# Optimization experiments

Measured on AMD Instinct MI355X. Metric: run time of the kernel, lower is better.

Reference implementation:

```python
import jax, jax.numpy as jnp
import numpy as np

N_NODES = 100000
N_EDGES = 3200000
IN_DIM = 128
OUT_DIM = 64
ITERS = 2


def setup_inputs() -> dict:
    key = jax.random.key(0)
    k1, k2, k3, k4, k5, k6 = jax.random.split(key, 6)
    feature = jax.random.normal(k1, (N_NODES, IN_DIM), dtype=jnp.float32)
    src = jax.random.randint(k2, (N_EDGES,), 0, N_NODES, dtype=jnp.int32)
    dst = jax.random.randint(k3, (N_EDGES,), 0, N_NODES, dtype=jnp.int32)
    # Kaiming-ish scaling for stability
    W_lin = jax.random.normal(k4, (IN_DIM, OUT_DIM), dtype=jnp.float32) / np.sqrt(IN_DIM)
    W_d1 = jax.random.normal(k5, (OUT_DIM, OUT_DIM), dtype=jnp.float32) / np.sqrt(OUT_DIM)
    W_d2 = jax.random.normal(k6, (OUT_DIM, OUT_DIM), dtype=jnp.float32) / np.sqrt(OUT_DIM)
    return {"feature": feature, "src": src, "dst": dst,
            "W_lin": W_lin, "W_d1": W_d1, "W_d2": W_d2}


def reference(feature, src, dst, W_lin, W_d1, W_d2):
    # u_i^0 = 0 ; u_i^j = tanh(linear(x_i) + dense(sum_{k in N(i)} u_k^{j-1}))
    base = feature @ W_lin                       # [N, OUT_DIM] (no bias)
    n = feature.shape[0]
    u = jnp.zeros((n, OUT_DIM), dtype=feature.dtype)
    for _ in range(ITERS):
        # copy_u + sum: message u[src] scattered-summed at dst
        m = jax.ops.segment_sum(u[src], dst, num_segments=n)   # [N, OUT_DIM]
        # Dense (2 layers, relu between, no bias): W_d2 @ relu(W_d1 @ m)
        h = jax.nn.relu(m @ W_d1) @ W_d2
        u = jnp.tanh(base + h)
    return u
```

## Files before the change

### kernel.cpp

```cpp
#include <hip/hip_runtime.h>
#include <math.h>

#define N_NODES 100000
#define N_EDGES 3200000
#define IN_DIM  128
#define OUT_DIM 64

#define BSHIFT   7
#define BNODES   128
#define NBUCKETS ((N_NODES + BNODES - 1) / BNODES)
#define NBINBLK  1024
#define CHUNK    (N_EDGES / NBINBLK)
#define SEGCAP   6144
#define MTILES   (N_NODES / 16)
#define GEMM_BLOCKS ((MTILES + 3) / 4)

typedef _Float16 half8 __attribute__((ext_vector_type(8)));
typedef float    f32x4 __attribute__((ext_vector_type(4)));

__device__ __forceinline__ int xcd_swz(int i) {
    return (i & 7) * (NBINBLK / 8) + (i >> 3);
}

__global__ __launch_bounds__(256) void fused_gemm_hist(
    const float* __restrict__ feature,
    const float* __restrict__ Wlin,
    float* __restrict__ base,
    _Float16* __restrict__ u1h,
    const int* __restrict__ dst,
    int* __restrict__ H)
{
    __shared__ int h[NBUCKETS];

    if (blockIdx.x < NBINBLK) {
        for (int k = threadIdx.x; k < NBUCKETS; k += 256) h[k] = 0;
        __syncthreads();

        int b = xcd_swz(blockIdx.x);
        int beg = b * CHUNK, end = beg + CHUNK;
        for (int i = beg + threadIdx.x; i < end; i += 256)
            atomicAdd(&h[dst[i] >> BSHIFT], 1);
        __syncthreads();

        for (int k = threadIdx.x; k < NBUCKETS; k += 256)
            H[(size_t)k * NBINBLK + b] = h[k];
        return;
    }

    int lane = threadIdx.x & 63;
    int wid  = ((blockIdx.x - NBINBLK) * 256 + threadIdx.x) >> 6;
    if (wid >= MTILES) return;

    int mrow = lane & 15;
    int kb   = lane >> 4;
    int k0   = kb * 8;

    half8 b[4][4];
#pragma unroll
    for (int s = 0; s < 4; ++s)
#pragma unroll
        for (int n = 0; n < 4; ++n)
#pragma unroll
            for (int j = 0; j < 8; ++j)
                b[s][n][j] = (_Float16)Wlin[(s * 32 + k0 + j) * OUT_DIM + n * 16 + mrow];

    int row = wid * 16 + mrow;
    const float4* fr = reinterpret_cast<const float4*>(feature + (size_t)row * IN_DIM);
    half8 a[4];
#pragma unroll
    for (int s = 0; s < 4; ++s) {
        float4 lo = fr[(s * 32 + k0) >> 2];
        float4 hi = fr[((s * 32 + k0) >> 2) + 1];
        a[s][0] = (_Float16)lo.x; a[s][1] = (_Float16)lo.y;
        a[s][2] = (_Float16)lo.z; a[s][3] = (_Float16)lo.w;
        a[s][4] = (_Float16)hi.x; a[s][5] = (_Float16)hi.y;
        a[s][6] = (_Float16)hi.z; a[s][7] = (_Float16)hi.w;
    }

    f32x4 acc[4];
#pragma unroll
    for (int n = 0; n < 4; ++n) acc[n] = (f32x4)0.f;

#pragma unroll
    for (int s = 0; s < 4; ++s)
#pragma unroll
        for (int n = 0; n < 4; ++n)
            acc[n] = __builtin_amdgcn_mfma_f32_16x16x32_f16(a[s], b[s][n], acc[n], 0, 0, 0);

#pragma unroll
    for (int n = 0; n < 4; ++n)
#pragma unroll
        for (int j = 0; j < 4; ++j) {
            int r = wid * 16 + kb * 4 + j;
            int c = n * 16 + mrow;
            float v = acc[n][j];
            base[(size_t)r * OUT_DIM + c] = v;
            u1h[(size_t)r * OUT_DIM + c] = (_Float16)tanhf(v);
        }
}

__global__ __launch_bounds__(NBINBLK) void scan_local(
    int* __restrict__ H, int* __restrict__ Btot)
{
    __shared__ int s[NBINBLK];
    int k = blockIdx.x, t = threadIdx.x;
    int v = H[(size_t)k * NBINBLK + t];
    s[t] = v;
    __syncthreads();
#pragma unroll
    for (int off = 1; off < NBINBLK; off <<= 1) {
        int x = (t >= off) ? s[t - off] : 0;
        __syncthreads();
        s[t] += x;
        __syncthreads();
    }
    H[(size_t)k * NBINBLK + t] = s[t] - v;
    if (t == NBINBLK - 1) Btot[k] = s[t];
}

__global__ __launch_bounds__(1024) void scan_tot(int* __restrict__ Btot)
{
    __shared__ int s[1024];
    int t = threadIdx.x;
    int v = (t < NBUCKETS) ? Btot[t] : 0;
    s[t] = v;
    __syncthreads();
#pragma unroll
    for (int off = 1; off < 1024; off <<= 1) {
        int x = (t >= off) ? s[t - off] : 0;
        __syncthreads();
        s[t] += x;
        __syncthreads();
    }
    if (t < NBUCKETS) Btot[t] = s[t] - v;
}

__global__ __launch_bounds__(512) void bin_scatter(
    const int* __restrict__ src,
    const int* __restrict__ dst,
    const int* __restrict__ H,
    const int* __restrict__ Btot,
    int* __restrict__ ebuf)
{
    __shared__ int cur[NBUCKETS];
    int b = xcd_swz(blockIdx.x);
    for (int k = threadIdx.x; k < NBUCKETS; k += 512)
        cur[k] = H[(size_t)k * NBINBLK + b] + Btot[k];
    __syncthreads();

    int beg = b * CHUNK, end = beg + CHUNK;
    for (int i = beg + threadIdx.x; i < end; i += 512) {
        int d = dst[i];
        int k = d >> BSHIFT;
        int p = atomicAdd(&cur[k], 1);
        ebuf[p] = src[i] | ((d & (BNODES - 1)) << 17);
    }
}

__global__ __launch_bounds__(512) void bucket_sort(
    const int* __restrict__ Btot,
    int* __restrict__ ebuf,
    int* __restrict__ node_off)
{
    __shared__ int seg[SEGCAP];
    __shared__ int cnt[BNODES];
    __shared__ int off[BNODES];
    int k = blockIdx.x;
    int beg = Btot[k];
    int end = (k + 1 < NBUCKETS) ? Btot[k + 1] : N_EDGES;
    int n = end - beg;

    for (int j = threadIdx.x; j < BNODES; j += 512) cnt[j] = 0;
    __syncthreads();

    for (int i = threadIdx.x; i < n; i += 512) {
        int v = ebuf[beg + i];
        seg[i] = v;
        atomicAdd(&cnt[v >> 17], 1);
    }
    __syncthreads();

    if (threadIdx.x == 0) {
        int node0 = k * BNODES;
        int nvalid = N_NODES - node0; if (nvalid > BNODES) nvalid = BNODES;
        int excl = 0;
        for (int j = 0; j < nvalid; ++j) {
            off[j] = excl;
            node_off[node0 + j] = beg + excl;
            excl += cnt[j];
        }
        if (k == NBUCKETS - 1) node_off[N_NODES] = end;
    }
    __syncthreads();

    for (int i = threadIdx.x; i < n; i += 512) {
        int v = seg[i];
        int p = atomicAdd(&off[v >> 17], 1);
        ebuf[beg + p] = v & 0x1FFFF;
    }
}

__global__ __launch_bounds__(256) void node_gather(
    const int* __restrict__ node_off,
    const int* __restrict__ csr,
    const half8* __restrict__ u1v,
    float* __restrict__ m)
{
    int wid = (blockIdx.x * 256 + threadIdx.x) >> 6;
    if (wid >= N_NODES) return;
    int lane = threadIdx.x & 63;
    int q = lane >> 3, c = lane & 7;

    int beg = node_off[wid];
    int end = node_off[wid + 1];
    int cnt = end - beg;
    int per = (cnt + 7) >> 3;
    int gb  = beg + q * per;
    int ge  = gb + per; if (ge > end) ge = end;

    float acc[8];
#pragma unroll
    for (int i = 0; i < 8; ++i) acc[i] = 0.f;

    int e = gb;
    for (; e + 4 <= ge; e += 4) {
        int s0 = csr[e];
        int s1 = csr[e + 1];
        int s2 = csr[e + 2];
        int s3 = csr[e + 3];
        half8 a = u1v[(size_t)s0 * 8 + c];
        half8 b = u1v[(size_t)s1 * 8 + c];
        half8 g = u1v[(size_t)s2 * 8 + c];
        half8 d = u1v[(size_t)s3 * 8 + c];
#pragma unroll
        for (int i = 0; i < 8; ++i)
            acc[i] += ((float)a[i] + (float)b[i]) + ((float)g[i] + (float)d[i]);
    }
    for (; e < ge; ++e) {
        half8 a = u1v[(size_t)csr[e] * 8 + c];
#pragma unroll
        for (int i = 0; i < 8; ++i) acc[i] += (float)a[i];
    }

#pragma unroll
    for (int i = 0; i < 8; ++i) {
        acc[i] += __shfl_xor(acc[i], 8);
        acc[i] += __shfl_xor(acc[i], 16);
        acc[i] += __shfl_xor(acc[i], 32);
    }

    if (q == 0) {
        float4* mr = reinterpret_cast<float4*>(m + (size_t)wid * OUT_DIM + c * 8);
        mr[0] = make_float4(acc[0], acc[1], acc[2], acc[3]);
        mr[1] = make_float4(acc[4], acc[5], acc[6], acc[7]);
    }
}

__global__ __launch_bounds__(256) void dense_tanh(
    const float* __restrict__ m,
    const float* __restrict__ W1,
    const float* __restrict__ W2,
    const float* __restrict__ base,
    float* __restrict__ out)
{
    __shared__ _Float16 tl[4][16][72];
    int lane = threadIdx.x & 63;
    int w    = threadIdx.x >> 6;
    int wid  = (blockIdx.x * 256 + threadIdx.x) >> 6;
    if (wid >= MTILES) return;

    int mrow = lane & 15;
    int kb   = lane >> 4;
    int k0   = kb * 8;

    half8 b1[2][4], b2[2][4];
#pragma unroll
    for (int s = 0; s < 2; ++s)
#pragma unroll
        for (int n = 0; n < 4; ++n)
#pragma unroll
            for (int j = 0; j < 8; ++j) {
                b1[s][n][j] = (_Float16)W1[(s * 32 + k0 + j) * 64 + n * 16 + mrow];
                b2[s][n][j] = (_Float16)W2[(s * 32 + k0 + j) * 64 + n * 16 + mrow];
            }

    int row = wid * 16 + mrow;
    const float4* mr = reinterpret_cast<const float4*>(m + (size_t)row * 64);
    half8 a[2];
#pragma unroll
    for (int s = 0; s < 2; ++s) {
        float4 lo = mr[(s * 32 + k0) >> 2];
        float4 hi = mr[((s * 32 + k0) >> 2) + 1];
        a[s][0] = (_Float16)lo.x; a[s][1] = (_Float16)lo.y;
        a[s][2] = (_Float16)lo.z; a[s][3] = (_Float16)lo.w;
        a[s][4] = (_Float16)hi.x; a[s][5] = (_Float16)hi.y;
        a[s][6] = (_Float16)hi.z; a[s][7] = (_Float16)hi.w;
    }

    f32x4 acc1[4];
#pragma unroll
    for (int n = 0; n < 4; ++n) acc1[n] = (f32x4)0.f;
#pragma unroll
    for (int s = 0; s < 2; ++s)
#pragma unroll
        for (int n = 0; n < 4; ++n)
            acc1[n] = __builtin_amdgcn_mfma_f32_16x16x32_f16(a[s], b1[s][n], acc1[n], 0, 0, 0);

#pragma unroll
    for (int n = 0; n < 4; ++n)
#pragma unroll
        for (int j = 0; j < 4; ++j)
            tl[w][kb * 4 + j][n * 16 + mrow] = (_Float16)fmaxf(acc1[n][j], 0.f);

    half8 a2[2];
#pragma unroll
    for (int s = 0; s < 2; ++s)
        a2[s] = *reinterpret_cast<const half8*>(&tl[w][mrow][s * 32 + k0]);

    f32x4 acc2[4];
#pragma unroll
    for (int n = 0; n < 4; ++n) acc2[n] = (f32x4)0.f;
#pragma unroll
    for (int s = 0; s < 2; ++s)
#pragma unroll
        for (int n = 0; n < 4; ++n)
            acc2[n] = __builtin_amdgcn_mfma_f32_16x16x32_f16(a2[s], b2[s][n], acc2[n], 0, 0, 0);

#pragma unroll
    for (int n = 0; n < 4; ++n)
#pragma unroll
        for (int j = 0; j < 4; ++j) {
            int r = wid * 16 + kb * 4 + j;
            int c = n * 16 + mrow;
            out[(size_t)r * 64 + c] = tanhf(base[(size_t)r * 64 + c] + acc2[n][j]);
        }
}

extern "C" void kernel_launch(void* const* d_in, const int* in_sizes, int n_in,
                              void* d_out, int out_size, void* d_ws, size_t ws_size,
                              hipStream_t stream)
{
    const float* feature = (const float*)d_in[0];
    const int*   src     = (const int*)d_in[1];
    const int*   dst     = (const int*)d_in[2];
    const float* W_lin   = (const float*)d_in[3];
    const float* W_d1    = (const float*)d_in[4];
    const float* W_d2    = (const float*)d_in[5];
    float* out = (float*)d_out;

    const size_t NODE_F = (size_t)N_NODES * OUT_DIM;

    float*    base     = (float*)d_ws;
    _Float16* u1h      = (_Float16*)(base + NODE_F);
    float*    m        = (float*)(u1h + NODE_F);
    int*      H        = (int*)(m + NODE_F);
    int*      Btot     = H + ((size_t)NBUCKETS * NBINBLK + 4);
    int*      node_off = Btot + (NBUCKETS + 4);
    int*      ebuf     = node_off + (N_NODES + 4);

    fused_gemm_hist<<<NBINBLK + GEMM_BLOCKS, 256, 0, stream>>>(
        feature, W_lin, base, u1h, dst, H);

    scan_local<<<NBUCKETS, NBINBLK, 0, stream>>>(H, Btot);
    scan_tot  <<<1, 1024, 0, stream>>>(Btot);
    bin_scatter<<<NBINBLK, 512, 0, stream>>>(src, dst, H, Btot, ebuf);
    bucket_sort<<<NBUCKETS, 512, 0, stream>>>(Btot, ebuf, node_off);

    int gather_blocks = (int)(((size_t)N_NODES * 64 + 255) / 256);
    node_gather<<<gather_blocks, 256, 0, stream>>>(
        node_off, ebuf, (const half8*)u1h, m);

    dense_tanh<<<GEMM_BLOCKS, 256, 0, stream>>>(m, W_d1, W_d2, base, out);
}
```

Measured before the change: 160.4 us.

## Fold bucket-total scan into consumers and store aggregated messages in fp16

Drops the single-block scan_tot kernel launch. Each block of bin_scatter and bucket_sort now recomputes the exclusive prefix of Btot redundantly in shared memory, trading extra per-block work and shared memory for one fewer serialized launch. Separately, node_gather writes the aggregated messages as fp16 half8 vectors instead of fp32. dense_tanh loads them directly as MFMA operands, which halves that intermediate's traffic and removes the conversion; the dense kernel already cast these values to fp16, but fp16 storage could overflow for large sums.

Measured after the change: 157.4 us. No clear change (-1.8%).

```diff
diff --git a/kernel.cpp b/kernel.cpp
--- a/kernel.cpp
+++ b/kernel.cpp
@@ -22,6 +22,38 @@
     return (i & 7) * (NBINBLK / 8) + (i >> 3);
 }
 
+__device__ __forceinline__ void scan_btot(
+    const int* __restrict__ Btot, int* bs, int* tmp)
+{
+    int t = threadIdx.x;
+    const int C = (NBUCKETS + 511) / 512;
+    int b0 = t * C;
+    int s = 0;
+#pragma unroll
+    for (int i = 0; i < C; ++i) {
+        int idx = b0 + i;
+        int v = (idx < NBUCKETS) ? Btot[idx] : 0;
+        if (idx < NBUCKETS) bs[idx] = v;
+        s += v;
+    }
+    tmp[t] = s;
+    __syncthreads();
+#pragma unroll
+    for (int o = 1; o < 512; o <<= 1) {
+        int v = (t >= o) ? tmp[t - o] : 0;
+        __syncthreads();
+        tmp[t] += v;
+        __syncthreads();
+    }
+    int excl = (t == 0) ? 0 : tmp[t - 1];
+#pragma unroll
+    for (int i = 0; i < C; ++i) {
+        int idx = b0 + i;
+        if (idx < NBUCKETS) { int v = bs[idx]; bs[idx] = excl; excl += v; }
+    }
+    __syncthreads();
+}
+
 __global__ __launch_bounds__(256) void fused_gemm_hist(
     const float* __restrict__ feature,
     const float* __restrict__ Wlin,
@@ -118,23 +150,6 @@
     if (t == NBINBLK - 1) Btot[k] = s[t];
 }
 
-__global__ __launch_bounds__(1024) void scan_tot(int* __restrict__ Btot)
-{
-    __shared__ int s[1024];
-    int t = threadIdx.x;
-    int v = (t < NBUCKETS) ? Btot[t] : 0;
-    s[t] = v;
-    __syncthreads();
-#pragma unroll
-    for (int off = 1; off < 1024; off <<= 1) {
-        int x = (t >= off) ? s[t - off] : 0;
-        __syncthreads();
-        s[t] += x;
-        __syncthreads();
-    }
-    if (t < NBUCKETS) Btot[t] = s[t] - v;
-}
-
 __global__ __launch_bounds__(512) void bin_scatter(
     const int* __restrict__ src,
     const int* __restrict__ dst,
@@ -143,9 +158,14 @@
     int* __restrict__ ebuf)
 {
     __shared__ int cur[NBUCKETS];
+    __shared__ int bs[NBUCKETS];
+    __shared__ int tmp[512];
+
+    scan_btot(Btot, bs, tmp);
+
     int b = xcd_swz(blockIdx.x);
     for (int k = threadIdx.x; k < NBUCKETS; k += 512)
-        cur[k] = H[(size_t)k * NBINBLK + b] + Btot[k];
+        cur[k] = H[(size_t)k * NBINBLK + b] + bs[k];
     __syncthreads();
 
     int beg = b * CHUNK, end = beg + CHUNK;
@@ -165,9 +185,14 @@
     __shared__ int seg[SEGCAP];
     __shared__ int cnt[BNODES];
     __shared__ int off[BNODES];
+    __shared__ int bs[NBUCKETS];
+    __shared__ int tmp[512];
+
+    scan_btot(Btot, bs, tmp);
+
     int k = blockIdx.x;
-    int beg = Btot[k];
-    int end = (k + 1 < NBUCKETS) ? Btot[k + 1] : N_EDGES;
+    int beg = bs[k];
+    int end = (k + 1 < NBUCKETS) ? bs[k + 1] : N_EDGES;
     int n = end - beg;
 
     for (int j = threadIdx.x; j < BNODES; j += 512) cnt[j] = 0;
@@ -204,7 +229,7 @@
     const int* __restrict__ node_off,
     const int* __restrict__ csr,
     const half8* __restrict__ u1v,
-    float* __restrict__ m)
+    half8* __restrict__ mh)
 {
     int wid = (blockIdx.x * 256 + threadIdx.x) >> 6;
     if (wid >= N_NODES) return;
@@ -250,14 +275,15 @@
     }
 
     if (q == 0) {
-        float4* mr = reinterpret_cast<float4*>(m + (size_t)wid * OUT_DIM + c * 8);
-        mr[0] = make_float4(acc[0], acc[1], acc[2], acc[3]);
-        mr[1] = make_float4(acc[4], acc[5], acc[6], acc[7]);
+        half8 hv;
+#pragma unroll
+        for (int i = 0; i < 8; ++i) hv[i] = (_Float16)acc[i];
+        mh[(size_t)wid * 8 + c] = hv;
     }
 }
 
 __global__ __launch_bounds__(256) void dense_tanh(
-    const float* __restrict__ m,
+    const half8* __restrict__ mh,
     const float* __restrict__ W1,
     const float* __restrict__ W2,
     const float* __restrict__ base,
@@ -285,17 +311,10 @@
             }
 
     int row = wid * 16 + mrow;
-    const float4* mr = reinterpret_cast<const float4*>(m + (size_t)row * 64);
     half8 a[2];
 #pragma unroll
-    for (int s = 0; s < 2; ++s) {
-        float4 lo = mr[(s * 32 + k0) >> 2];
-        float4 hi = mr[((s * 32 + k0) >> 2) + 1];
-        a[s][0] = (_Float16)lo.x; a[s][1] = (_Float16)lo.y;
-        a[s][2] = (_Float16)lo.z; a[s][3] = (_Float16)lo.w;
-        a[s][4] = (_Float16)hi.x; a[s][5] = (_Float16)hi.y;
-        a[s][6] = (_Float16)hi.z; a[s][7] = (_Float16)hi.w;
-    }
+    for (int s = 0; s < 2; ++s)
+        a[s] = mh[(size_t)row * 8 + ((s * 32 + k0) >> 3)];
 
     f32x4 acc1[4];
 #pragma unroll
@@ -352,8 +371,8 @@
 
     float*    base     = (float*)d_ws;
     _Float16* u1h      = (_Float16*)(base + NODE_F);
-    float*    m        = (float*)(u1h + NODE_F);
-    int*      H        = (int*)(m + NODE_F);
+    _Float16* mh       = u1h + NODE_F;
+    int*      H        = (int*)(mh + NODE_F);
     int*      Btot     = H + ((size_t)NBUCKETS * NBINBLK + 4);
     int*      node_off = Btot + (NBUCKETS + 4);
     int*      ebuf     = node_off + (N_NODES + 4);
@@ -362,13 +381,13 @@
         feature, W_lin, base, u1h, dst, H);
 
     scan_local<<<NBUCKETS, NBINBLK, 0, stream>>>(H, Btot);
-    scan_tot  <<<1, 1024, 0, stream>>>(Btot);
     bin_scatter<<<NBINBLK, 512, 0, stream>>>(src, dst, H, Btot, ebuf);
     bucket_sort<<<NBUCKETS, 512, 0, stream>>>(Btot, ebuf, node_off);
 
     int gather_blocks = (int)(((size_t)N_NODES * 64 + 255) / 256);
     node_gather<<<gather_blocks, 256, 0, stream>>>(
-        node_off, ebuf, (const half8*)u1h, m);
-
-    dense_tanh<<<GEMM_BLOCKS, 256, 0, stream>>>(m, W_d1, W_d2, base, out);
-}
+        node_off, ebuf, (const half8*)u1h, (half8*)mh);
+
+    dense_tanh<<<GEMM_BLOCKS, 256, 0, stream>>>(
+        (const half8*)mh, W_d1, W_d2, base, out);
+}
```
